# Performance work log

Hardware: AMD Instinct MI355X
Metric: run time of the kernel (lower is better)

## Reference

```python
import jax, jax.numpy as jnp
import numpy as np

C_, A_, B_ = 1, 128, 128          # image_size
H, Z, T, N = 512, 128, 16, 32     # h_dim, z_dim, steps, attention grid
EPS = 1e-8
BATCH = 256
PATCH = C_ * N * N                # read/write patch size (C_=1)
IN_ENC = 2 * PATCH + H


def gru_cell(x, h, W_ih, W_hh, b_ih, b_hh):
    gi = x @ W_ih.T + b_ih
    gh = h @ W_hh.T + b_hh
    i_r, i_z, i_n = jnp.split(gi, 3, axis=-1)
    h_r, h_z, h_n = jnp.split(gh, 3, axis=-1)
    r = jax.nn.sigmoid(i_r + h_r)
    z = jax.nn.sigmoid(i_z + h_z)
    n = jnp.tanh(i_n + r * h_n)
    return (1.0 - z) * n + z * h


def filterbank(gt, delta, two_sigma_sq, num_pixels):
    # gt, delta: [b,1]; two_sigma_sq: [b,1,1]
    g = 0.5 * (num_pixels + 1) * (gt + 1.0)                       # [b,1]
    grid = jnp.arange(N, dtype=jnp.float32) - 0.5 * (N - 1)       # [N]
    mu = g + grid[None, :] * delta                                # [b,N]
    pix = jnp.arange(num_pixels, dtype=jnp.float32)               # [P]
    F = jnp.exp(-(pix[None, None, :] - mu[:, :, None]) ** 2 / two_sigma_sq)
    return F / jnp.maximum(F.sum(axis=-1, keepdims=True), EPS)    # [b,N,P]


def get_filterbanks(h_dec, W_attn, b_attn):
    p = h_dec @ W_attn.T + b_attn                                 # [b,5]
    gt_x, gt_y, log_ss, log_dt, log_g = [p[:, i:i + 1] for i in range(5)]
    two_sigma_sq = (2.0 * jnp.exp(log_ss))[:, :, None]            # [b,1,1]
    delta = (max(A_, B_) - 1) * jnp.exp(log_dt) / (N - 1)         # [b,1]
    gamma = jnp.exp(log_g)                                        # [b,1]
    F_x = filterbank(gt_x, delta, two_sigma_sq, A_)               # [b,N,A]
    F_y = filterbank(gt_y, delta, two_sigma_sq, B_)               # [b,N,B]
    return F_x, F_y, gamma


def draw_forward(x, eps, W_ih_enc, W_hh_enc, b_ih_enc, b_hh_enc,
                 W_ih_dec, W_hh_dec, b_ih_dec, b_hh_dec,
                 W_mu, b_mu, W_ls, b_ls, W_wr, b_wr,
                 W_ra, b_ra, W_wa, b_wa):
    b = x.shape[0]
    xf = x.reshape(b, -1)                                         # [b, A*B]
    reconsts0 = jnp.zeros_like(xf)
    h0 = jnp.zeros((b, H), dtype=xf.dtype)

    def step(carry, eps_t):
        reconsts, h_enc, h_dec = carry
        # NOTE: faithful to original: reconsts[-1] is last batch row, broadcast
        x_hat = xf - jax.nn.sigmoid(reconsts[-1])
        # ---- read with attention ----
        F_x, F_y, gamma = get_filterbanks(h_dec, W_ra, b_ra)
        F_x_t = jnp.swapaxes(F_x, -1, -2)                         # [b,A,N]
        img = xf.reshape(b, A_, B_)
        img_hat = x_hat.reshape(b, A_, B_)
        x_attn = (F_y @ img @ F_x_t).reshape(b, -1)               # [b,N*N]
        xh_attn = (F_y @ img_hat @ F_x_t).reshape(b, -1)
        r = gamma * jnp.concatenate([x_attn, xh_attn], axis=1)    # [b,2*N*N]
        # ---- encoder GRU ----
        h_enc = gru_cell(jnp.concatenate([r, h_dec], axis=1), h_enc,
                         W_ih_enc, W_hh_enc, b_ih_enc, b_hh_enc)
        # ---- sample z ~ Q ----
        mu = h_enc @ W_mu.T + b_mu
        sigma = jnp.exp(h_enc @ W_ls.T + b_ls)
        z = mu + eps_t * sigma
        # ---- decoder GRU ----
        h_dec = gru_cell(z, h_dec, W_ih_dec, W_hh_dec, b_ih_dec, b_hh_dec)
        # ---- write with attention ----
        F_xw, F_yw, gamma_w = get_filterbanks(h_dec, W_wa, b_wa)
        w = (h_dec @ W_wr.T + b_wr).reshape(b, N, N)
        wr = (jnp.swapaxes(F_yw, -1, -2) @ w @ F_xw).reshape(b, -1) / gamma_w
        return (reconsts + wr, h_enc, h_dec), None

    (reconsts, _, _), _ = jax.lax.scan(step, (reconsts0, h0, h0), eps)
    return jax.nn.sigmoid(reconsts).reshape(-1, C_, A_, B_)


def setup_inputs() -> dict:
    key = jax.random.key(0)
    ks = jax.random.split(key, 24)
    s = 0.02
    inp = {
        "x": jax.random.uniform(ks[0], (BATCH, C_, A_, B_), jnp.float32),
        "eps": jax.random.normal(ks[1], (T, BATCH, Z), jnp.float32),
        "W_ih_enc": jax.random.normal(ks[2], (3 * H, IN_ENC), jnp.float32) * s,
        "W_hh_enc": jax.random.normal(ks[3], (3 * H, H), jnp.float32) * s,
        "b_ih_enc": jnp.zeros((3 * H,), jnp.float32),
        "b_hh_enc": jnp.zeros((3 * H,), jnp.float32),
        "W_ih_dec": jax.random.normal(ks[4], (3 * H, Z), jnp.float32) * s,
        "W_hh_dec": jax.random.normal(ks[5], (3 * H, H), jnp.float32) * s,
        "b_ih_dec": jnp.zeros((3 * H,), jnp.float32),
        "b_hh_dec": jnp.zeros((3 * H,), jnp.float32),
        "W_mu": jax.random.normal(ks[6], (Z, H), jnp.float32) * s,
        "b_mu": jnp.zeros((Z,), jnp.float32),
        "W_ls": jax.random.normal(ks[7], (Z, H), jnp.float32) * s,
        "b_ls": jnp.zeros((Z,), jnp.float32),
        "W_wr": jax.random.normal(ks[8], (PATCH, H), jnp.float32) * s,
        "b_wr": jnp.zeros((PATCH,), jnp.float32),
        "W_ra": jax.random.normal(ks[9], (5, H), jnp.float32) * s,
        "b_ra": jnp.zeros((5,), jnp.float32),
        "W_wa": jax.random.normal(ks[10], (5, H), jnp.float32) * s,
        "b_wa": jnp.zeros((5,), jnp.float32),
    }
    return inp


def reference(x, eps, W_ih_enc, W_hh_enc, b_ih_enc, b_hh_enc,
              W_ih_dec, W_hh_dec, b_ih_dec, b_hh_dec,
              W_mu, b_mu, W_ls, b_ls, W_wr, b_wr,
              W_ra, b_ra, W_wa, b_wa):
    return draw_forward(x, eps, W_ih_enc, W_hh_enc, b_ih_enc, b_hh_enc,
                        W_ih_dec, W_hh_dec, b_ih_dec, b_hh_dec,
                        W_mu, b_mu, W_ls, b_ls, W_wr, b_wr,
                        W_ra, b_ra, W_wa, b_wa)
```

## Files before the change

### kernel.cpp

```cpp
#include <hip/hip_runtime.h>
#include <math.h>

#define BATCHN 256
#define HDIM 512
#define ZDIM 128
#define NGRID 32
#define ABDIM 128
#define IMGSZ 16384
#define ENCIN 2560
#define G3 1536
#define SLAB (BATCHN*G3)

typedef __attribute__((ext_vector_type(8))) short short8;
typedef __attribute__((ext_vector_type(4))) float f32x4;

__device__ __forceinline__ float sigmoidf_(float x){ return 1.0f/(1.0f+expf(-x)); }

__device__ __forceinline__ ushort f2bf_rne(float f){
    union{float f; uint u;} x; x.f=f;
    uint r = (x.u + 0x7FFFu + ((x.u>>16)&1u)) >> 16;
    return (ushort)r;
}
__device__ __forceinline__ float bf2f(ushort h){
    union{uint u; float f;} y; y.u = ((uint)h)<<16;
    return y.f;
}

__global__ void init_slast_k(float* __restrict__ s_last){
    int i = blockIdx.x*256 + threadIdx.x;
    s_last[i] = 0.5f;
}

__global__ void conv_wh_k(const float* __restrict__ W, ushort* __restrict__ Wh, int n4){
    int i = blockIdx.x*256 + threadIdx.x;
    if(i>=n4) return;
    float4 v = ((const float4*)W)[i];
    ushort4 hv;
    hv.x=f2bf_rne(v.x); hv.y=f2bf_rne(v.y); hv.z=f2bf_rne(v.z); hv.w=f2bf_rne(v.w);
    ((ushort4*)Wh)[i] = hv;
}

__device__ __forceinline__ void stage_swz(const ushort* __restrict__ g, int K,
        int grow0, int kb, ushort* lds, int tid){
    int wv = tid>>6, lane = tid&63;
    #pragma unroll
    for(int q=0;q<2;q++){
        int instr = wv*2 + q;
        int rl = instr*8 + (lane>>3);
        int sc = (lane&7) ^ (lane>>3);
        const ushort* src = g + (size_t)(grow0+rl)*K + kb + sc*8;
        ushort* dst = lds + instr*512;
        __builtin_amdgcn_global_load_lds((const __attribute__((address_space(1))) void*)src,
                                         (__attribute__((address_space(3))) void*)dst, 16, 0, 0);
    }
}

__device__ __forceinline__ short8 lds_read_swz(const ushort* arr, int r, int slot){
    return *(const short8*)&arr[r*64 + ((slot ^ (r&7))<<3)];
}

__device__ __forceinline__ void attn_params_dev512(const float* __restrict__ h,
        const float* __restrict__ W, const float* __restrict__ bvec,
        float* red5, float* pp, int tid){
    float accp[5];
    #pragma unroll
    for(int i=0;i<5;i++) accp[i]=0.f;
    for(int k=tid;k<HDIM;k+=512){
        float hv = h[k];
        #pragma unroll
        for(int i=0;i<5;i++) accp[i] += hv*W[i*HDIM+k];
    }
    int wv = tid>>6;
    #pragma unroll
    for(int i=0;i<5;i++){
        float a = accp[i];
        #pragma unroll
        for(int o=32;o>0;o>>=1) a += __shfl_down(a,o);
        if((tid&63)==0) red5[i*8+wv]=a;
    }
    __syncthreads();
    if(tid<5){
        float s = bvec[tid];
        #pragma unroll
        for(int w2=0;w2<8;w2++) s += red5[tid*8+w2];
        pp[tid]=s;
    }
    __syncthreads();
}

__device__ __forceinline__ void fill_fb_T(float* fxT, float* fyT, const float* pp, int tid){
    float gx = 64.5f*(pp[0]+1.0f);
    float gy = 64.5f*(pp[1]+1.0f);
    float tss = 2.0f*expf(pp[2]);
    float delta = (127.0f/31.0f)*expf(pp[3]);
    int rr = tid>>3;
    int q  = tid&7;
    int j  = rr&31;
    bool isY = rr>=32;
    float mu = (isY?gy:gx) + ((float)j-15.5f)*delta;
    float v[16]; float s=0.f;
    #pragma unroll
    for(int i=0;i<16;i++){
        float d = (float)(q*16+i)-mu;
        float e = expf(-d*d/tss);
        v[i]=e; s+=e;
    }
    s += __shfl_xor(s,1); s += __shfl_xor(s,2); s += __shfl_xor(s,4);
    float inv = 1.0f/fmaxf(s,1e-8f);
    float* dst = isY? fyT : fxT;
    #pragma unroll
    for(int i=0;i<16;i++) dst[(q*16+i)*32 + j] = v[i]*inv;
    __syncthreads();
}

__device__ __forceinline__ void fill_fb_R(float (*fx)[ABDIM+1], float (*fy)[ABDIM+1], const float* pp, int tid){
    float gx = 64.5f*(pp[0]+1.0f);
    float gy = 64.5f*(pp[1]+1.0f);
    float tss = 2.0f*expf(pp[2]);
    float delta = (127.0f/31.0f)*expf(pp[3]);
    int rr = tid>>3;
    int q  = tid&7;
    int j  = rr&31;
    bool isY = rr>=32;
    float mu = (isY?gy:gx) + ((float)j-15.5f)*delta;
    float v[16]; float s=0.f;
    #pragma unroll
    for(int i=0;i<16;i++){
        float d = (float)(q*16+i)-mu;
        float e = expf(-d*d/tss);
        v[i]=e; s+=e;
    }
    s += __shfl_xor(s,1); s += __shfl_xor(s,2); s += __shfl_xor(s,4);
    float inv = 1.0f/fmaxf(s,1e-8f);
    float* rowp = isY? &fy[j][0] : &fx[j][0];
    #pragma unroll
    for(int i=0;i<16;i++) rowp[q*16+i] = v[i]*inv;
    __syncthreads();
}

__global__ __launch_bounds__(512) void read_attn_k(const float* __restrict__ xf, const float* __restrict__ s_last,
        const float* __restrict__ hdec, const ushort* __restrict__ Hd_h, const ushort* __restrict__ Hd_l,
        const float* __restrict__ W_ra, const float* __restrict__ b_ra,
        ushort* __restrict__ Eh, ushort* __restrict__ El){
    __shared__ float smem[4096 + 8256 + 48];
    float* sFxT = smem;
    float* sFyT = smem + 4096;
    float* tmp  = smem + 4096;
    float* red5 = smem + 4096 + 8256;
    float* pp   = red5 + 40;
    int bb = blockIdx.x; int tid = threadIdx.x;
    const float* h = hdec + bb*HDIM;
    attn_params_dev512(h, W_ra, b_ra, red5, pp, tid);
    float gamma = expf(pp[4]);
    fill_fb_T(sFxT, sFyT, pp, tid);

    const float* img = xf + (size_t)bb*IMGSZ;
    int c = tid & 127;
    int jg = tid >> 7;
    float acc0[8], accS[8];
    #pragma unroll
    for(int i=0;i<8;i++){ acc0[i]=0.f; accS[i]=0.f; }
    for(int k=0;k<ABDIM;k++){
        float s  = img[k*ABDIM + c];
        float sl = s_last[k*ABDIM + c];
        float4 f0 = *(const float4*)&sFyT[k*32 + jg*8];
        float4 f1 = *(const float4*)&sFyT[k*32 + jg*8 + 4];
        acc0[0]+=f0.x*s;  acc0[1]+=f0.y*s;  acc0[2]+=f0.z*s;  acc0[3]+=f0.w*s;
        acc0[4]+=f1.x*s;  acc0[5]+=f1.y*s;  acc0[6]+=f1.z*s;  acc0[7]+=f1.w*s;
        accS[0]+=f0.x*sl; accS[1]+=f0.y*sl; accS[2]+=f0.z*sl; accS[3]+=f0.w*sl;
        accS[4]+=f1.x*sl; accS[5]+=f1.y*sl; accS[6]+=f1.z*sl; accS[7]+=f1.w*sl;
    }
    __syncthreads();
    #pragma unroll
    for(int i=0;i<8;i++){
        int j = jg*8+i;
        tmp[0*32*129 + j*129 + c] = acc0[i];
        tmp[1*32*129 + j*129 + c] = acc0[i] - accS[i];
    }
    __syncthreads();
    {
        int i4 = tid & 7;
        int j  = (tid>>3) & 31;
        int p  = tid >> 8;
        float a0=0.f,a1=0.f,a2=0.f,a3=0.f;
        for(int cc=0; cc<ABDIM; cc++){
            float tv = tmp[p*32*129 + j*129 + cc];
            float4 fx = *(const float4*)&sFxT[cc*32 + i4*4];
            a0 += tv*fx.x; a1 += tv*fx.y; a2 += tv*fx.z; a3 += tv*fx.w;
        }
        float ov[4] = {gamma*a0, gamma*a1, gamma*a2, gamma*a3};
        ushort4 oh, ol; ushort hq;
        hq=f2bf_rne(ov[0]); oh.x=hq; ol.x=f2bf_rne(ov[0]-bf2f(hq));
        hq=f2bf_rne(ov[1]); oh.y=hq; ol.y=f2bf_rne(ov[1]-bf2f(hq));
        hq=f2bf_rne(ov[2]); oh.z=hq; ol.z=f2bf_rne(ov[2]-bf2f(hq));
        hq=f2bf_rne(ov[3]); oh.w=hq; ol.w=f2bf_rne(ov[3]-bf2f(hq));
        size_t off = (size_t)bb*ENCIN + p*1024 + j*NGRID + i4*4;
        *(ushort4*)(Eh + off) = oh;
        *(ushort4*)(El + off) = ol;
    }
    {
        int i = tid;
        Eh[(size_t)bb*ENCIN + 2048 + i] = Hd_h[(size_t)bb*HDIM + i];
        El[(size_t)bb*ENCIN + 2048 + i] = Hd_l[(size_t)bb*HDIM + i];
    }
}

__device__ void gemm_one(const ushort* __restrict__ Agh, const ushort* __restrict__ Agl,
        const ushort* __restrict__ Wh,
        int K, int k0, int kiters, int row0, int col0, int Nn, float* __restrict__ Out,
        ushort* AH, ushort* AL, ushort* BH, int tid){
    int lane = tid&63, w = tid>>6;
    int m0 = (w>>1)*32, n0 = (w&1)*32;
    int fr = lane&15, sl = lane>>4;
    f32x4 acc[2][2];
    #pragma unroll
    for(int i=0;i<2;i++)
        #pragma unroll
        for(int j=0;j<2;j++) acc[i][j]=(f32x4){0.f,0.f,0.f,0.f};
    for(int it=0; it<kiters; ++it){
        int kb = k0 + it*64;
        stage_swz(Agh, K, row0, kb, AH, tid);
        stage_swz(Agl, K, row0, kb, AL, tid);
        stage_swz(Wh,  K, col0, kb, BH, tid);
        __syncthreads();
        #pragma unroll
        for(int ks=0; ks<2; ks++){
            int slot = ks*4 + sl;
            short8 a_h[2], a_l[2], b_h[2];
            #pragma unroll
            for(int mf=0;mf<2;mf++){
                a_h[mf] = lds_read_swz(AH, m0+mf*16+fr, slot);
                a_l[mf] = lds_read_swz(AL, m0+mf*16+fr, slot);
            }
            #pragma unroll
            for(int nf=0;nf<2;nf++)
                b_h[nf] = lds_read_swz(BH, n0+nf*16+fr, slot);
            #pragma unroll
            for(int mf=0;mf<2;mf++)
                #pragma unroll
                for(int nf=0;nf<2;nf++){
                    acc[mf][nf] = __builtin_amdgcn_mfma_f32_16x16x32_bf16(a_h[mf], b_h[nf], acc[mf][nf], 0,0,0);
                    acc[mf][nf] = __builtin_amdgcn_mfma_f32_16x16x32_bf16(a_l[mf], b_h[nf], acc[mf][nf], 0,0,0);
                }
        }
        __syncthreads();
    }
    int crow = (lane>>4)*4, ccol = lane&15;
    #pragma unroll
    for(int mf=0;mf<2;mf++)
        #pragma unroll
        for(int nf=0;nf<2;nf++)
            #pragma unroll
            for(int r=0;r<4;r++)
                Out[(size_t)(row0+m0+mf*16+crow+r)*Nn + col0+n0+nf*16+ccol] = acc[mf][nf][r];
}

__global__ __launch_bounds__(256) void gemm3_k(
        const ushort* __restrict__ Eh, const ushort* __restrict__ El,
        const ushort* __restrict__ Wie_h,
        const ushort* __restrict__ He_h, const ushort* __restrict__ He_l,
        const ushort* __restrict__ Whe_h,
        const ushort* __restrict__ Hd_h, const ushort* __restrict__ Hd_l,
        const ushort* __restrict__ Whd_h,
        float* __restrict__ Pi, float* __restrict__ Ph, float* __restrict__ Ph2){
    __shared__ ushort AH[64*64], AL[64*64], BH[64*64];
    int job = blockIdx.x, tid = threadIdx.x;
    if(job < 384){
        int tile = job % 96, s = job / 96;
        gemm_one(Eh, El, Wie_h, ENCIN, s*640, 10,
                 (tile/24)*64, (tile%24)*64, G3, Pi + (size_t)s*SLAB, AH, AL, BH, tid);
    } else if(job < 480){
        int tile = job - 384;
        gemm_one(He_h, He_l, Whe_h, HDIM, 0, 8,
                 (tile/24)*64, (tile%24)*64, G3, Ph, AH, AL, BH, tid);
    } else {
        int tile = job - 480;
        gemm_one(Hd_h, Hd_l, Whd_h, HDIM, 0, 8,
                 (tile/24)*64, (tile%24)*64, G3, Ph2, AH, AL, BH, tid);
    }
}

__global__ __launch_bounds__(256) void gemm_wr_k(
        const ushort* __restrict__ Hd_h, const ushort* __restrict__ Hd_l,
        const ushort* __restrict__ Wwr_h,
        float* __restrict__ Pw){
    __shared__ ushort AH[64*64], AL[64*64], BH[64*64];
    int tid = threadIdx.x;
    int r0 = blockIdx.y*64, c0 = blockIdx.x*64, s = blockIdx.z;
    gemm_one(Hd_h, Hd_l, Wwr_h, HDIM, s*128, 2, r0, c0, 1024,
             Pw + (size_t)s*BATCHN*1024, AH, AL, BH, tid);
}

__global__ __launch_bounds__(512) void combine_z_k(const float* __restrict__ Pi, const float* __restrict__ Ph,
        const float* __restrict__ bi, const float* __restrict__ bh,
        float* __restrict__ h, ushort* __restrict__ Hh, ushort* __restrict__ Hl,
        const float* __restrict__ Wmu, const float* __restrict__ bmu,
        const float* __restrict__ Wls, const float* __restrict__ bls,
        const float* __restrict__ eps_t, ushort* __restrict__ Zh, ushort* __restrict__ Zl){
    __shared__ float hs[HDIM];
    int bb = blockIdx.x, tid = threadIdx.x;
    int j = tid;
    float gi_r=bi[j], gi_z=bi[512+j], gi_n=bi[1024+j];
    float gh_r=bh[j], gh_z=bh[512+j], gh_n=bh[1024+j];
    #pragma unroll
    for(int s=0;s<4;s++){
        size_t base = (size_t)s*SLAB + (size_t)bb*G3 + j;
        gi_r += Pi[base]; gi_z += Pi[base+512]; gi_n += Pi[base+1024];
    }
    {
        size_t base = (size_t)bb*G3 + j;
        gh_r += Ph[base]; gh_z += Ph[base+512]; gh_n += Ph[base+1024];
    }
    float r = sigmoidf_(gi_r + gh_r);
    float z = sigmoidf_(gi_z + gh_z);
    float n = tanhf(gi_n + r*gh_n);
    size_t hoff = (size_t)bb*HDIM + j;
    float hn = (1.f - z)*n + z*h[hoff];
    h[hoff] = hn; hs[j] = hn;
    ushort hh = f2bf_rne(hn);
    Hh[hoff] = hh; Hl[hoff] = f2bf_rne(hn - bf2f(hh));
    __syncthreads();
    {
        int wv = tid>>6, lane = tid&63;
        const float4* hs4 = (const float4*)hs;
        float4 h0 = hs4[lane*2];
        float4 h1 = hs4[lane*2+1];
        #pragma unroll 4
        for(int it=0; it<16; ++it){
            int jo = wv*16 + it;
            const float4* wm = (const float4*)(Wmu + (size_t)jo*HDIM);
            const float4* wl = (const float4*)(Wls + (size_t)jo*HDIM);
            float4 m0=wm[lane*2], m1=wm[lane*2+1];
            float4 l0=wl[lane*2], l1=wl[lane*2+1];
            float am  = h0.x*m0.x+h0.y*m0.y+h0.z*m0.z+h0.w*m0.w
                      + h1.x*m1.x+h1.y*m1.y+h1.z*m1.z+h1.w*m1.w;
            float al_ = h0.x*l0.x+h0.y*l0.y+h0.z*l0.z+h0.w*l0.w
                      + h1.x*l1.x+h1.y*l1.y+h1.z*l1.z+h1.w*l1.w;
            #pragma unroll
            for(int o=32;o>0;o>>=1){ am += __shfl_down(am,o); al_ += __shfl_down(al_,o); }
            if(lane==0){
                float mu = am + bmu[jo];
                float sg = expf(al_ + bls[jo]);
                float zv = mu + eps_t[(size_t)bb*ZDIM + jo]*sg;
                ushort zh = f2bf_rne(zv);
                Zh[(size_t)bb*ZDIM + jo] = zh;
                Zl[(size_t)bb*ZDIM + jo] = f2bf_rne(zv - bf2f(zh));
            }
        }
    }
}

__global__ __launch_bounds__(256) void deci_combine_k(
        const ushort* __restrict__ Zh, const ushort* __restrict__ Zl,
        const ushort* __restrict__ Wid_h,
        const float* __restrict__ Ph2, const float* __restrict__ bi, const float* __restrict__ bh,
        float* __restrict__ h, ushort* __restrict__ Hh, ushort* __restrict__ Hl){
    __shared__ ushort AH[64*64], AL[64*64], BH[64*64];
    int tid = threadIdx.x;
    int lane = tid&63, w = tid>>6;
    int m0 = (w>>1)*32, n0 = (w&1)*32;
    int fr = lane&15, sl = lane>>4;
    int row0 = blockIdx.y*64;
    int jcol0 = blockIdx.x*64;
    f32x4 acc[3][2][2];
    #pragma unroll
    for(int g=0;g<3;g++)
        #pragma unroll
        for(int i=0;i<2;i++)
            #pragma unroll
            for(int jj=0;jj<2;jj++) acc[g][i][jj]=(f32x4){0.f,0.f,0.f,0.f};
    for(int it=0; it<2; ++it){
        int kb = it*64;
        stage_swz(Zh, ZDIM, row0, kb, AH, tid);
        stage_swz(Zl, ZDIM, row0, kb, AL, tid);
        for(int g=0; g<3; ++g){
            stage_swz(Wid_h, ZDIM, g*512 + jcol0, kb, BH, tid);
            __syncthreads();
            #pragma unroll
            for(int ks=0; ks<2; ks++){
                int slot = ks*4 + sl;
                short8 a_h[2], a_l[2], b_h[2];
                #pragma unroll
                for(int mf=0;mf<2;mf++){
                    a_h[mf] = lds_read_swz(AH, m0+mf*16+fr, slot);
                    a_l[mf] = lds_read_swz(AL, m0+mf*16+fr, slot);
                }
                #pragma unroll
                for(int nf=0;nf<2;nf++)
                    b_h[nf] = lds_read_swz(BH, n0+nf*16+fr, slot);
                #pragma unroll
                for(int mf=0;mf<2;mf++)
                    #pragma unroll
                    for(int nf=0;nf<2;nf++){
                        acc[g][mf][nf] = __builtin_amdgcn_mfma_f32_16x16x32_bf16(a_h[mf], b_h[nf], acc[g][mf][nf], 0,0,0);
                        acc[g][mf][nf] = __builtin_amdgcn_mfma_f32_16x16x32_bf16(a_l[mf], b_h[nf], acc[g][mf][nf], 0,0,0);
                    }
            }
            __syncthreads();
        }
    }
    int crow = (lane>>4)*4, ccol = lane&15;
    #pragma unroll
    for(int mf=0;mf<2;mf++)
        #pragma unroll
        for(int nf=0;nf<2;nf++)
            #pragma unroll
            for(int r=0;r<4;r++){
                int row = row0 + m0 + mf*16 + crow + r;
                int col = jcol0 + n0 + nf*16 + ccol;
                size_t pbase = (size_t)row*G3 + col;
                float gi_r = acc[0][mf][nf][r] + bi[col];
                float gi_z = acc[1][mf][nf][r] + bi[512+col];
                float gi_n = acc[2][mf][nf][r] + bi[1024+col];
                float gh_r = Ph2[pbase]      + bh[col];
                float gh_z = Ph2[pbase+512]  + bh[512+col];
                float gh_n = Ph2[pbase+1024] + bh[1024+col];
                float rr = sigmoidf_(gi_r + gh_r);
                float zz = sigmoidf_(gi_z + gh_z);
                float nn = tanhf(gi_n + rr*gh_n);
                size_t idx = (size_t)row*HDIM + col;
                float hn = (1.f - zz)*nn + zz*h[idx];
                h[idx] = hn;
                ushort hh = f2bf_rne(hn);
                Hh[idx] = hh; Hl[idx] = f2bf_rne(hn - bf2f(hh));
            }
}

__global__ __launch_bounds__(512) void write_apply_k(const float* __restrict__ Pw, const float* __restrict__ b_wr,
        const float* __restrict__ hdec, const float* __restrict__ W_wa, const float* __restrict__ b_wa,
        float* __restrict__ rec, float* __restrict__ s_last, int last){
    __shared__ float sFy[NGRID][ABDIM+1];
    __shared__ float sFx[NGRID][ABDIM+1];
    __shared__ float sw[NGRID][36];
    __shared__ float t[ABDIM][36];
    __shared__ float red5[40];
    __shared__ float pp[8];
    int bb = blockIdx.x, tid = threadIdx.x;
    const float* h = hdec + bb*HDIM;
    attn_params_dev512(h, W_wa, b_wa, red5, pp, tid);
    float invg = expf(-pp[4]);
    fill_fb_R(sFx, sFy, pp, tid);
    for(int i=tid;i<NGRID*NGRID;i+=512){
        float a = b_wr[i];
        #pragma unroll
        for(int s=0;s<4;s++) a += Pw[((size_t)s*BATCHN + bb)*1024 + i];
        sw[i>>5][i&31] = a;
    }
    __syncthreads();
    {
        int p = tid>>2, iq = tid&3;
        float a[8];
        #pragma unroll
        for(int i=0;i<8;i++) a[i]=0.f;
        for(int j=0;j<NGRID;j++){
            float fy = sFy[j][p];
            float4 w0 = *(const float4*)&sw[j][iq*8];
            float4 w1 = *(const float4*)&sw[j][iq*8+4];
            a[0]+=fy*w0.x; a[1]+=fy*w0.y; a[2]+=fy*w0.z; a[3]+=fy*w0.w;
            a[4]+=fy*w1.x; a[5]+=fy*w1.y; a[6]+=fy*w1.z; a[7]+=fy*w1.w;
        }
        float4 o0; o0.x=a[0];o0.y=a[1];o0.z=a[2];o0.w=a[3];
        float4 o1; o1.x=a[4];o1.y=a[5];o1.z=a[6];o1.w=a[7];
        *(float4*)&t[p][iq*8]   = o0;
        *(float4*)&t[p][iq*8+4] = o1;
    }
    __syncthreads();
    {
        int q = tid&127, pg = tid>>7;
        float fxc[32];
        #pragma unroll
        for(int i=0;i<32;i++) fxc[i] = sFx[i][q];
        for(int pi=0; pi<32; pi++){
            int p = pg*32 + pi;
            float acc = 0.f;
            #pragma unroll
            for(int i4=0;i4<8;i4++){
                float4 tv = *(const float4*)&t[p][i4*4];
                acc += tv.x*fxc[i4*4] + tv.y*fxc[i4*4+1] + tv.z*fxc[i4*4+2] + tv.w*fxc[i4*4+3];
            }
            size_t off = (size_t)bb*IMGSZ + p*ABDIM + q;
            float nv = rec[off] + acc*invg;
            rec[off] = last ? sigmoidf_(nv) : nv;
            if(bb==BATCHN-1) s_last[p*ABDIM + q] = sigmoidf_(nv);
        }
    }
}

extern "C" void kernel_launch(void* const* d_in, const int* in_sizes, int n_in,
                              void* d_out, int out_size, void* d_ws, size_t ws_size,
                              hipStream_t stream) {
    const float* x        = (const float*)d_in[0];
    const float* eps      = (const float*)d_in[1];
    const float* W_ih_enc = (const float*)d_in[2];
    const float* W_hh_enc = (const float*)d_in[3];
    const float* b_ih_enc = (const float*)d_in[4];
    const float* b_hh_enc = (const float*)d_in[5];
    const float* W_ih_dec = (const float*)d_in[6];
    const float* W_hh_dec = (const float*)d_in[7];
    const float* b_ih_dec = (const float*)d_in[8];
    const float* b_hh_dec = (const float*)d_in[9];
    const float* W_mu     = (const float*)d_in[10];
    const float* b_mu     = (const float*)d_in[11];
    const float* W_ls     = (const float*)d_in[12];
    const float* b_ls     = (const float*)d_in[13];
    const float* W_wr     = (const float*)d_in[14];
    const float* b_wr     = (const float*)d_in[15];
    const float* W_ra     = (const float*)d_in[16];
    const float* b_ra     = (const float*)d_in[17];
    const float* W_wa     = (const float*)d_in[18];
    const float* b_wa     = (const float*)d_in[19];

    float* rec = (float*)d_out;

    float* ws = (float*)d_ws;
    float* h_enc  = ws;  ws += BATCHN*HDIM;
    float* h_dec  = ws;  ws += BATCHN*HDIM;
    float* s_last = ws;  ws += IMGSZ;
    float* Pi     = ws;  ws += (size_t)4*SLAB;
    float* Ph     = ws;  ws += (size_t)SLAB;
    float* Ph2    = ws;  ws += (size_t)SLAB;
    float* Pw     = ws;  ws += (size_t)4*BATCHN*1024;

    ushort* us = (ushort*)ws;
    ushort* Wie_h = us; us += 1536*2560;
    ushort* Whe_h = us; us += 1536*512;
    ushort* Whd_h = us; us += 1536*512;
    ushort* Wid_h = us; us += 1536*128;
    ushort* Wwr_h = us; us += 1024*512;
    ushort* Eh    = us; us += BATCHN*ENCIN;
    ushort* El    = us; us += BATCHN*ENCIN;
    ushort* He_h  = us; us += BATCHN*HDIM;
    ushort* He_l  = us; us += BATCHN*HDIM;
    ushort* Hd_h  = us; us += BATCHN*HDIM;
    ushort* Hd_l  = us; us += BATCHN*HDIM;
    ushort* Zh    = us; us += BATCHN*ZDIM;
    ushort* Zl    = us; us += BATCHN*ZDIM;

    hipMemsetAsync(rec,   0, (size_t)BATCHN*IMGSZ*sizeof(float), stream);
    hipMemsetAsync(h_enc, 0, (size_t)BATCHN*HDIM*sizeof(float), stream);
    hipMemsetAsync(h_dec, 0, (size_t)BATCHN*HDIM*sizeof(float), stream);
    hipMemsetAsync(He_h,  0, (size_t)BATCHN*HDIM*sizeof(ushort)*2, stream);
    hipMemsetAsync(Hd_h,  0, (size_t)BATCHN*HDIM*sizeof(ushort)*2, stream);
    init_slast_k<<<IMGSZ/256,256,0,stream>>>(s_last);

    conv_wh_k<<<(1536*2560/4+255)/256,256,0,stream>>>(W_ih_enc, Wie_h, 1536*2560/4);
    conv_wh_k<<<(1536*512/4+255)/256,256,0,stream>>>(W_hh_enc, Whe_h, 1536*512/4);
    conv_wh_k<<<(1536*512/4+255)/256,256,0,stream>>>(W_hh_dec, Whd_h, 1536*512/4);
    conv_wh_k<<<(1536*128/4+255)/256,256,0,stream>>>(W_ih_dec, Wid_h, 1536*128/4);
    conv_wh_k<<<(1024*512/4+255)/256,256,0,stream>>>(W_wr, Wwr_h, 1024*512/4);

    for(int t=0;t<16;t++){
        read_attn_k<<<BATCHN,512,0,stream>>>(x, s_last, h_dec, Hd_h, Hd_l, W_ra, b_ra, Eh, El);
        gemm3_k<<<576,256,0,stream>>>(Eh, El, Wie_h, He_h, He_l, Whe_h,
                                      Hd_h, Hd_l, Whd_h, Pi, Ph, Ph2);
        combine_z_k<<<BATCHN,512,0,stream>>>(Pi, Ph, b_ih_enc, b_hh_enc,
            h_enc, He_h, He_l, W_mu, b_mu, W_ls, b_ls, eps + (size_t)t*BATCHN*ZDIM, Zh, Zl);
        deci_combine_k<<<dim3(8,4),256,0,stream>>>(Zh, Zl, Wid_h, Ph2,
            b_ih_dec, b_hh_dec, h_dec, Hd_h, Hd_l);
        gemm_wr_k<<<dim3(16,4,4),256,0,stream>>>(Hd_h, Hd_l, Wwr_h, Pw);
        write_apply_k<<<BATCHN,512,0,stream>>>(Pw, b_wr, h_dec, W_wa, b_wa, rec, s_last,
                                               (t==15)?1:0);
    }
}
```

Baseline: 1.376 ms.

## Split read/write attention per image across two blocks; halve write GEMM split-K

The read and write attention kernels now launch two blocks per batch image, each handling half the glimpse rows (read) or half the output image rows (write). This doubles the block count from 256 to 512 to fill more compute units. The cost is that each block recomputes the attention parameters and filterbanks, and the read kernel streams the full image twice. Separately, the write-patch GEMM drops from a 4-way to a 2-way K split, so there are fewer partial buffers to sum but fewer blocks run in that GEMM.

```diff
diff --git a/kernel.cpp b/kernel.cpp
--- a/kernel.cpp
+++ b/kernel.cpp
@@ -148,7 +148,8 @@
     float* tmp  = smem + 4096;
     float* red5 = smem + 4096 + 8256;
     float* pp   = red5 + 40;
-    int bb = blockIdx.x; int tid = threadIdx.x;
+    int bb = blockIdx.x >> 1, half = blockIdx.x & 1;
+    int tid = threadIdx.x;
     const float* h = hdec + bb*HDIM;
     attn_params_dev512(h, W_ra, b_ra, red5, pp, tid);
     float gamma = expf(pp[4]);
@@ -157,48 +158,45 @@
     const float* img = xf + (size_t)bb*IMGSZ;
     int c = tid & 127;
     int jg = tid >> 7;
-    float acc0[8], accS[8];
-    #pragma unroll
-    for(int i=0;i<8;i++){ acc0[i]=0.f; accS[i]=0.f; }
+    int jbase = half*16 + jg*4;
+    float acc0[4], accS[4];
+    #pragma unroll
+    for(int i=0;i<4;i++){ acc0[i]=0.f; accS[i]=0.f; }
     for(int k=0;k<ABDIM;k++){
         float s  = img[k*ABDIM + c];
         float sl = s_last[k*ABDIM + c];
-        float4 f0 = *(const float4*)&sFyT[k*32 + jg*8];
-        float4 f1 = *(const float4*)&sFyT[k*32 + jg*8 + 4];
+        float4 f0 = *(const float4*)&sFyT[k*32 + jbase];
         acc0[0]+=f0.x*s;  acc0[1]+=f0.y*s;  acc0[2]+=f0.z*s;  acc0[3]+=f0.w*s;
-        acc0[4]+=f1.x*s;  acc0[5]+=f1.y*s;  acc0[6]+=f1.z*s;  acc0[7]+=f1.w*s;
         accS[0]+=f0.x*sl; accS[1]+=f0.y*sl; accS[2]+=f0.z*sl; accS[3]+=f0.w*sl;
-        accS[4]+=f1.x*sl; accS[5]+=f1.y*sl; accS[6]+=f1.z*sl; accS[7]+=f1.w*sl;
-    }
-    __syncthreads();
-    #pragma unroll
-    for(int i=0;i<8;i++){
-        int j = jg*8+i;
-        tmp[0*32*129 + j*129 + c] = acc0[i];
-        tmp[1*32*129 + j*129 + c] = acc0[i] - accS[i];
+    }
+    __syncthreads();
+    #pragma unroll
+    for(int i=0;i<4;i++){
+        int jl = jg*4+i;
+        tmp[0*16*129 + jl*129 + c] = acc0[i];
+        tmp[1*16*129 + jl*129 + c] = acc0[i] - accS[i];
     }
     __syncthreads();
     {
-        int i4 = tid & 7;
-        int j  = (tid>>3) & 31;
+        int i2 = tid & 15;
+        int jl = (tid>>4) & 15;
         int p  = tid >> 8;
-        float a0=0.f,a1=0.f,a2=0.f,a3=0.f;
+        float a0=0.f, a1=0.f;
         for(int cc=0; cc<ABDIM; cc++){
-            float tv = tmp[p*32*129 + j*129 + cc];
-            float4 fx = *(const float4*)&sFxT[cc*32 + i4*4];
-            a0 += tv*fx.x; a1 += tv*fx.y; a2 += tv*fx.z; a3 += tv*fx.w;
+            float tv = tmp[p*16*129 + jl*129 + cc];
+            a0 += tv*sFxT[cc*32 + i2*2];
+            a1 += tv*sFxT[cc*32 + i2*2 + 1];
         }
-        float ov[4] = {gamma*a0, gamma*a1, gamma*a2, gamma*a3};
-        ushort4 oh, ol; ushort hq;
-        hq=f2bf_rne(ov[0]); oh.x=hq; ol.x=f2bf_rne(ov[0]-bf2f(hq));
-        hq=f2bf_rne(ov[1]); oh.y=hq; ol.y=f2bf_rne(ov[1]-bf2f(hq));
-        hq=f2bf_rne(ov[2]); oh.z=hq; ol.z=f2bf_rne(ov[2]-bf2f(hq));
-        hq=f2bf_rne(ov[3]); oh.w=hq; ol.w=f2bf_rne(ov[3]-bf2f(hq));
-        size_t off = (size_t)bb*ENCIN + p*1024 + j*NGRID + i4*4;
-        *(ushort4*)(Eh + off) = oh;
-        *(ushort4*)(El + off) = ol;
-    }
-    {
+        float o0 = gamma*a0, o1 = gamma*a1;
+        int j = half*16 + jl;
+        ushort h0=f2bf_rne(o0), h1=f2bf_rne(o1);
+        ushort2 oh; oh.x=h0; oh.y=h1;
+        ushort2 ol; ol.x=f2bf_rne(o0-bf2f(h0)); ol.y=f2bf_rne(o1-bf2f(h1));
+        size_t off = (size_t)bb*ENCIN + p*1024 + j*NGRID + i2*2;
+        *(ushort2*)(Eh + off) = oh;
+        *(ushort2*)(El + off) = ol;
+    }
+    if(half==0){
         int i = tid;
         Eh[(size_t)bb*ENCIN + 2048 + i] = Hd_h[(size_t)bb*HDIM + i];
         El[(size_t)bb*ENCIN + 2048 + i] = Hd_l[(size_t)bb*HDIM + i];
@@ -287,7 +285,7 @@
     __shared__ ushort AH[64*64], AL[64*64], BH[64*64];
     int tid = threadIdx.x;
     int r0 = blockIdx.y*64, c0 = blockIdx.x*64, s = blockIdx.z;
-    gemm_one(Hd_h, Hd_l, Wwr_h, HDIM, s*128, 2, r0, c0, 1024,
+    gemm_one(Hd_h, Hd_l, Wwr_h, HDIM, s*256, 4, r0, c0, 1024,
              Pw + (size_t)s*BATCHN*1024, AH, AL, BH, tid);
 }
 
@@ -432,10 +430,12 @@
     __shared__ float sFy[NGRID][ABDIM+1];
     __shared__ float sFx[NGRID][ABDIM+1];
     __shared__ float sw[NGRID][36];
-    __shared__ float t[ABDIM][36];
+    __shared__ float t[64][36];
     __shared__ float red5[40];
     __shared__ float pp[8];
-    int bb = blockIdx.x, tid = threadIdx.x;
+    int bb = blockIdx.x >> 1, half = blockIdx.x & 1;
+    int p0 = half*64;
+    int tid = threadIdx.x;
     const float* h = hdec + bb*HDIM;
     attn_params_dev512(h, W_wa, b_wa, red5, pp, tid);
     float invg = expf(-pp[4]);
@@ -443,26 +443,23 @@
     for(int i=tid;i<NGRID*NGRID;i+=512){
         float a = b_wr[i];
         #pragma unroll
-        for(int s=0;s<4;s++) a += Pw[((size_t)s*BATCHN + bb)*1024 + i];
+        for(int s=0;s<2;s++) a += Pw[((size_t)s*BATCHN + bb)*1024 + i];
         sw[i>>5][i&31] = a;
     }
     __syncthreads();
     {
-        int p = tid>>2, iq = tid&3;
-        float a[8];
-        #pragma unroll
-        for(int i=0;i<8;i++) a[i]=0.f;
+        int pl = tid>>3, iq = tid&7;
+        int p = p0 + pl;
+        float a[4];
+        #pragma unroll
+        for(int i=0;i<4;i++) a[i]=0.f;
         for(int j=0;j<NGRID;j++){
             float fy = sFy[j][p];
-            float4 w0 = *(const float4*)&sw[j][iq*8];
-            float4 w1 = *(const float4*)&sw[j][iq*8+4];
+            float4 w0 = *(const float4*)&sw[j][iq*4];
             a[0]+=fy*w0.x; a[1]+=fy*w0.y; a[2]+=fy*w0.z; a[3]+=fy*w0.w;
-            a[4]+=fy*w1.x; a[5]+=fy*w1.y; a[6]+=fy*w1.z; a[7]+=fy*w1.w;
         }
         float4 o0; o0.x=a[0];o0.y=a[1];o0.z=a[2];o0.w=a[3];
-        float4 o1; o1.x=a[4];o1.y=a[5];o1.z=a[6];o1.w=a[7];
-        *(float4*)&t[p][iq*8]   = o0;
-        *(float4*)&t[p][iq*8+4] = o1;
+        *(float4*)&t[pl][iq*4] = o0;
     }
     __syncthreads();
     {
@@ -470,12 +467,13 @@
         float fxc[32];
         #pragma unroll
         for(int i=0;i<32;i++) fxc[i] = sFx[i][q];
-        for(int pi=0; pi<32; pi++){
-            int p = pg*32 + pi;
+        for(int pi=0; pi<16; pi++){
+            int pl = pg*16 + pi;
+            int p = p0 + pl;
             float acc = 0.f;
             #pragma unroll
             for(int i4=0;i4<8;i4++){
-                float4 tv = *(const float4*)&t[p][i4*4];
+                float4 tv = *(const float4*)&t[pl][i4*4];
                 acc += tv.x*fxc[i4*4] + tv.y*fxc[i4*4+1] + tv.z*fxc[i4*4+2] + tv.w*fxc[i4*4+3];
             }
             size_t off = (size_t)bb*IMGSZ + p*ABDIM + q;
@@ -519,7 +517,7 @@
     float* Pi     = ws;  ws += (size_t)4*SLAB;
     float* Ph     = ws;  ws += (size_t)SLAB;
     float* Ph2    = ws;  ws += (size_t)SLAB;
-    float* Pw     = ws;  ws += (size_t)4*BATCHN*1024;
+    float* Pw     = ws;  ws += (size_t)2*BATCHN*1024;
 
     ushort* us = (ushort*)ws;
     ushort* Wie_h = us; us += 1536*2560;
@@ -550,15 +548,15 @@
     conv_wh_k<<<(1024*512/4+255)/256,256,0,stream>>>(W_wr, Wwr_h, 1024*512/4);
 
     for(int t=0;t<16;t++){
-        read_attn_k<<<BATCHN,512,0,stream>>>(x, s_last, h_dec, Hd_h, Hd_l, W_ra, b_ra, Eh, El);
+        read_attn_k<<<2*BATCHN,512,0,stream>>>(x, s_last, h_dec, Hd_h, Hd_l, W_ra, b_ra, Eh, El);
         gemm3_k<<<576,256,0,stream>>>(Eh, El, Wie_h, He_h, He_l, Whe_h,
                                       Hd_h, Hd_l, Whd_h, Pi, Ph, Ph2);
         combine_z_k<<<BATCHN,512,0,stream>>>(Pi, Ph, b_ih_enc, b_hh_enc,
             h_enc, He_h, He_l, W_mu, b_mu, W_ls, b_ls, eps + (size_t)t*BATCHN*ZDIM, Zh, Zl);
         deci_combine_k<<<dim3(8,4),256,0,stream>>>(Zh, Zl, Wid_h, Ph2,
             b_ih_dec, b_hh_dec, h_dec, Hd_h, Hd_l);
-        gemm_wr_k<<<dim3(16,4,4),256,0,stream>>>(Hd_h, Hd_l, Wwr_h, Pw);
-        write_apply_k<<<BATCHN,512,0,stream>>>(Pw, b_wr, h_dec, W_wa, b_wa, rec, s_last,
-                                               (t==15)?1:0);
-    }
-}
+        gemm_wr_k<<<dim3(16,4,2),256,0,stream>>>(Hd_h, Hd_l, Wwr_h, Pw);
+        write_apply_k<<<2*BATCHN,512,0,stream>>>(Pw, b_wr, h_dec, W_wa, b_wa, rec, s_last,
+                                                 (t==15)?1:0);
+    }
+}
```

Result: no change. 1.377 ms (+0.0%).
